# Kernel tuning notes

Hardware: AMD Instinct MI355X
Metric: run time of the kernel (lower is better)

## Reference

```python
import jax, jax.numpy as jnp
import numpy as np

N = 100000
DIM = 128
E_A = 500000
E_D = 500000


def setup_inputs() -> dict:
    key = jax.random.key(0)
    ks = jax.random.split(key, 8)
    h = jax.random.normal(ks[0], (N, DIM), dtype=jnp.float32)
    a_idx = jax.random.randint(ks[1], (E_A, 3), 0, N, dtype=jnp.int64 if jax.config.jax_enable_x64 else jnp.int32)
    a_val = jax.random.uniform(ks[2], (E_A, 1), dtype=jnp.float32)
    d_idx = jax.random.randint(ks[3], (E_D, 4), 0, N, dtype=jnp.int64 if jax.config.jax_enable_x64 else jnp.int32)
    d_val = jax.random.uniform(ks[4], (E_D, 1), dtype=jnp.float32)
    # Linear weights stored as [in, out]; init ~ Kaiming-uniform-ish scale
    W_a = jax.random.normal(ks[5], (3 * DIM + 1, DIM), dtype=jnp.float32) * (1.0 / np.sqrt(3 * DIM + 1))
    b_a = jnp.zeros((DIM,), dtype=jnp.float32)
    W_d = jax.random.normal(ks[6], (4 * DIM + 1, DIM), dtype=jnp.float32) * (1.0 / np.sqrt(4 * DIM + 1))
    b_d = jnp.zeros((DIM,), dtype=jnp.float32)
    W_h = jax.random.normal(ks[7], (3 * DIM, DIM), dtype=jnp.float32) * (1.0 / np.sqrt(3 * DIM))
    b_h = jnp.zeros((DIM,), dtype=jnp.float32)
    return {"h": h, "a_idx": a_idx, "a_val": a_val, "d_idx": d_idx, "d_val": d_val,
            "W_a": W_a, "b_a": b_a, "W_d": W_d, "b_d": b_d, "W_h": W_h, "b_h": b_h}


def reference(h, a_idx, a_val, d_idx, d_val, W_a, b_a, W_d, b_d, W_h, b_h):
    n = h.shape[0]
    # angle messages: gather 3 node embeddings + scalar, Linear + SiLU, scatter to center node
    x_a = jnp.concatenate([h[a_idx[:, 0]], h[a_idx[:, 1]], h[a_idx[:, 2]], a_val], axis=-1)  # [E_a, 3d+1]
    m_ijk = jax.nn.silu(x_a @ W_a + b_a)  # [E_a, d]
    agg_a = jax.ops.segment_sum(m_ijk, a_idx[:, 1], num_segments=n)  # [N, d]
    # dihedral messages: gather 4 node embeddings + scalar
    x_d = jnp.concatenate([h[d_idx[:, 0]], h[d_idx[:, 1]], h[d_idx[:, 2]], h[d_idx[:, 3]], d_val], axis=-1)  # [E_d, 4d+1]
    m_ijkl = jax.nn.silu(x_d @ W_d + b_d)  # [E_d, d]
    agg_d = jax.ops.segment_sum(m_ijkl, d_idx[:, 1], num_segments=n)  # [N, d]
    # residual node update
    return h + jnp.concatenate([h, agg_a, agg_d], axis=-1) @ W_h + b_h
```

## Files before the change

### kernel.cpp

```cpp
#include <hip/hip_runtime.h>
#include <hip/hip_bf16.h>

#define DIM 128
#define LDS_STRIDE 136
#define SC_STRIDE 132

typedef __attribute__((ext_vector_type(8))) __bf16 bf16x8;
typedef __attribute__((ext_vector_type(4))) __bf16 bf16x4;
typedef __attribute__((ext_vector_type(2))) __bf16 bf16x2;
typedef __attribute__((ext_vector_type(4))) float f32x4;

__global__ __launch_bounds__(256) void prep_w(const float* __restrict__ W_a,
                                              const float* __restrict__ W_d,
                                              const float* __restrict__ W_h,
                                              __bf16* __restrict__ Wt)
{
    int idx = blockIdx.x * 256 + threadIdx.x;
    if (idx >= 10 * 16384) return;
    int t   = idx >> 14;
    int rem = idx & 16383;
    int c   = rem >> 7;
    int k   = rem & 127;
    const float* src;
    if (t < 3)      src = W_a + (size_t)t * 16384;
    else if (t < 7) src = W_d + (size_t)(t - 3) * 16384;
    else            src = W_h + (size_t)(t - 7) * 16384;
    Wt[(size_t)t * 16384 + c * 128 + k] = (__bf16)src[k * 128 + c];
}

__device__ __forceinline__ void stage_wt(const __bf16* __restrict__ Wtj,
                                         __bf16 (*sB)[LDS_STRIDE], int tid)
{
    for (int it = 0; it < 8; ++it) {
        int idx = tid + it * 256;
        int c  = idx >> 4;
        int k8 = (idx & 15) << 3;
        *(bf16x8*)&sB[c][k8] = *(const bf16x8*)(Wtj + c * 128 + k8);
    }
}

__device__ __forceinline__ void load_afrag_f32(const float* __restrict__ src,
                                               int row, int lk, int N, bf16x8 afrag[4])
{
    const float* rp = src + (size_t)row * DIM;
    #pragma unroll
    for (int ks = 0; ks < 4; ++ks) {
        float4 v0 = make_float4(0.f, 0.f, 0.f, 0.f), v1 = v0;
        if (row < N) {
            v0 = *(const float4*)(rp + ks * 32 + lk);
            v1 = *(const float4*)(rp + ks * 32 + lk + 4);
        }
        bf16x8 a;
        a[0] = (__bf16)v0.x; a[1] = (__bf16)v0.y; a[2] = (__bf16)v0.z; a[3] = (__bf16)v0.w;
        a[4] = (__bf16)v1.x; a[5] = (__bf16)v1.y; a[6] = (__bf16)v1.z; a[7] = (__bf16)v1.w;
        afrag[ks] = a;
    }
}

__device__ __forceinline__ void load_afrag_bf16(const __bf16* __restrict__ src,
                                                int row, int lk, int N, bf16x8 afrag[4])
{
    const __bf16* rp = src + (size_t)row * DIM;
    #pragma unroll
    for (int ks = 0; ks < 4; ++ks) {
        bf16x8 a = {};
        if (row < N) a = *(const bf16x8*)(rp + ks * 32 + lk);
        afrag[ks] = a;
    }
}

__global__ __launch_bounds__(256, 4) void proj(const float* __restrict__ src,
                                               const __bf16* __restrict__ Wt,
                                               __bf16* __restrict__ dst,
                                               int N)
{
    __shared__ __bf16 sB[128][LDS_STRIDE];
    float* sC = reinterpret_cast<float*>(sB);
    const int tid = threadIdx.x;
    const int j = blockIdx.y;
    const int node0 = blockIdx.x * 64;
    const int wave = tid >> 6, lane = tid & 63;
    const int lrow = lane & 15;
    const int lk   = (lane >> 4) * 8;
    const int arow = node0 + wave * 16 + lrow;

    stage_wt(Wt + (size_t)j * 16384, sB, tid);

    bf16x8 afrag[4];
    load_afrag_f32(src, arow, lk, N, afrag);
    __syncthreads();

    f32x4 acc[8];
    #pragma unroll
    for (int ct = 0; ct < 8; ++ct) acc[ct] = (f32x4){0.f, 0.f, 0.f, 0.f};

    #pragma unroll
    for (int ks = 0; ks < 4; ++ks) {
        int k0 = ks * 32 + lk;
        #pragma unroll
        for (int ct = 0; ct < 8; ++ct) {
            bf16x8 b = *(const bf16x8*)&sB[ct * 16 + lrow][k0];
            acc[ct] = __builtin_amdgcn_mfma_f32_16x16x32_bf16(afrag[ks], b, acc[ct], 0, 0, 0);
        }
    }

    __syncthreads();
    {
        int rbase = wave * 16 + (lane >> 4) * 4;
        #pragma unroll
        for (int r = 0; r < 4; ++r)
            #pragma unroll
            for (int ct = 0; ct < 8; ++ct)
                sC[(rbase + r) * SC_STRIDE + ct * 16 + lrow] = acc[ct][r];
    }
    __syncthreads();

    __bf16* dj = dst + (size_t)j * N * DIM;
    for (int it = 0; it < 8; ++it) {
        int idx = tid + it * 256;
        int row = idx >> 5;
        int c4  = (idx & 31) << 2;
        int grow = node0 + row;
        if (grow < N) {
            const float* sp = sC + row * SC_STRIDE + c4;
            bf16x4 o;
            o[0] = (__bf16)sp[0]; o[1] = (__bf16)sp[1];
            o[2] = (__bf16)sp[2]; o[3] = (__bf16)sp[3];
            *(bf16x4*)(dj + (size_t)grow * DIM + c4) = o;
        }
    }
}

__global__ __launch_bounds__(256) void csr_count_both(const int* __restrict__ a_idx,
                                                      const int* __restrict__ d_idx,
                                                      int* __restrict__ offs,
                                                      int EA, int ED, int N)
{
    int e = blockIdx.x * 256 + threadIdx.x;
    if (e < EA) {
        atomicAdd(&offs[a_idx[3 * (size_t)e + 1]], 1);
    } else if (e < EA + ED) {
        int k = e - EA;
        atomicAdd(&offs[N + d_idx[4 * (size_t)k + 1]], 1);
    }
}

#define SCAN_CHUNK 1024

__global__ __launch_bounds__(256) void scan_s1(int* __restrict__ data,
                                               int* __restrict__ partials, int n)
{
    __shared__ int lds[256];
    const int t = threadIdx.x;
    const int base = blockIdx.x * SCAN_CHUNK + t * 4;
    int v[4];
    #pragma unroll
    for (int i = 0; i < 4; ++i) v[i] = (base + i < n) ? data[base + i] : 0;
    int tsum = v[0] + v[1] + v[2] + v[3];
    lds[t] = tsum; __syncthreads();
    for (int off = 1; off < 256; off <<= 1) {
        int x = (t >= off) ? lds[t - off] : 0;
        __syncthreads();
        lds[t] += x;
        __syncthreads();
    }
    if (t == 255) partials[blockIdx.x] = lds[255];
    int run = lds[t] - tsum;
    #pragma unroll
    for (int i = 0; i < 4; ++i) {
        int nv = run; run += v[i];
        if (base + i < n) data[base + i] = nv;
    }
}

__global__ __launch_bounds__(256) void scan_s2(int* __restrict__ partials, int nb)
{
    __shared__ int lds[256];
    const int t = threadIdx.x;
    int v = (t < nb) ? partials[t] : 0;
    lds[t] = v; __syncthreads();
    for (int off = 1; off < 256; off <<= 1) {
        int x = (t >= off) ? lds[t - off] : 0;
        __syncthreads();
        lds[t] += x;
        __syncthreads();
    }
    if (t < nb) partials[t] = lds[t] - v;
}

__global__ __launch_bounds__(256) void scan_s3(int* __restrict__ data,
                                               const int* __restrict__ partials, int n)
{
    const int add = partials[blockIdx.x];
    const int base = blockIdx.x * SCAN_CHUNK + threadIdx.x * 4;
    #pragma unroll
    for (int i = 0; i < 4; ++i)
        if (base + i < n) data[base + i] += add;
}

__global__ __launch_bounds__(256) void csr_fill_both(const int* __restrict__ a_idx,
                                                     const float* __restrict__ a_val,
                                                     const int* __restrict__ d_idx,
                                                     const float* __restrict__ d_val,
                                                     int* __restrict__ offs,
                                                     int4* __restrict__ recs,
                                                     int EA, int ED, int N)
{
    int e = blockIdx.x * 256 + threadIdx.x;
    if (e < EA) {
        int i0 = a_idx[3 * (size_t)e + 0];
        int i1 = a_idx[3 * (size_t)e + 1];
        int i2 = a_idx[3 * (size_t)e + 2];
        int slot = atomicAdd(&offs[i1], 1);
        recs[slot] = make_int4(i0 * 256, i2 * 256, __float_as_int(a_val[e]), 0);
    } else if (e < EA + ED) {
        int k = e - EA;
        int i0 = d_idx[4 * (size_t)k + 0];
        int i1 = d_idx[4 * (size_t)k + 1];
        int i2 = d_idx[4 * (size_t)k + 2];
        int i3 = d_idx[4 * (size_t)k + 3];
        int slot = atomicAdd(&offs[N + i1], 1);
        recs[slot] = make_int4(i0 * 256, i2 * 256, i3 * 256, __float_as_int(d_val[k]));
    }
}

__device__ __forceinline__ float silu(float x) { return x / (1.f + __expf(-x)); }

__global__ __launch_bounds__(256) void gather3(const __bf16* __restrict__ P,
                                               const float* __restrict__ wlast,
                                               const float* __restrict__ bias,
                                               const int* __restrict__ offs,
                                               const int4* __restrict__ recs,
                                               float* __restrict__ aggf, int N)
{
    const int tid = threadIdx.x;
    const int n = blockIdx.x * 4 + (tid >> 6);
    if (n >= N) return;
    const int lane = tid & 63;
    const int half = lane >> 5;
    const int gl = lane & 31;
    const int f  = gl * 4;
    const int fb = gl * 8;
    const size_t NBb = (size_t)N * DIM * 2;
    const char* P0b = (const char*)P;
    const char* P1b = P0b + NBb;
    const char* P2b = P0b + 2 * NBb;
    int start = (n == 0) ? 0 : offs[n - 1];
    int end = offs[n];

    float wl[4], base[4];
    {
        const float* wp = wlast + f;
        const float* bp = bias + f;
        bf16x4 p1 = *(const bf16x4*)(P1b + (size_t)n * 256 + fb);
        #pragma unroll
        for (int c = 0; c < 4; ++c) { wl[c] = wp[c]; base[c] = (float)p1[c] + bp[c]; }
    }
    float a[4] = {0.f, 0.f, 0.f, 0.f};

    const int cnt = end - start;
    const int npair = cnt >> 1;
    int s = start;
    for (int p = 0; p < npair; ++p, s += 2) {
        int4 r = recs[s + half];
        bf16x4 q0 = *(const bf16x4*)(P0b + r.x + fb);
        bf16x4 q2 = *(const bf16x4*)(P2b + r.y + fb);
        float v = __int_as_float(r.z);
        #pragma unroll
        for (int c = 0; c < 4; ++c)
            a[c] += silu((float)q0[c] + (float)q2[c] + v * wl[c] + base[c]);
    }
    if (cnt & 1) {
        int4 r = recs[end - 1];
        bf16x4 q0 = *(const bf16x4*)(P0b + r.x + fb);
        bf16x4 q2 = *(const bf16x4*)(P2b + r.y + fb);
        float v = __int_as_float(r.z);
        if (half == 0) {
            #pragma unroll
            for (int c = 0; c < 4; ++c)
                a[c] += silu((float)q0[c] + (float)q2[c] + v * wl[c] + base[c]);
        }
    }
    #pragma unroll
    for (int c = 0; c < 4; ++c) a[c] += __shfl_xor(a[c], 32, 64);
    if (half == 0) {
        f32x4 o;
        #pragma unroll
        for (int c = 0; c < 4; ++c) o[c] = a[c];
        *(f32x4*)(aggf + (size_t)n * DIM + f) = o;
    }
}

__global__ __launch_bounds__(256) void gather4(const __bf16* __restrict__ P,
                                               const float* __restrict__ wlast,
                                               const float* __restrict__ bias,
                                               const int* __restrict__ offs_d,
                                               const int4* __restrict__ recs,
                                               __bf16* __restrict__ agg, int N)
{
    const int tid = threadIdx.x;
    const int n = blockIdx.x * 4 + (tid >> 6);
    if (n >= N) return;
    const int lane = tid & 63;
    const int half = lane >> 5;
    const int gl = lane & 31;
    const int f  = gl * 4;
    const int fb = gl * 8;
    const size_t NBb = (size_t)N * DIM * 2;
    const char* P0b = (const char*)P;
    const char* P1b = P0b + NBb;
    const char* P2b = P0b + 2 * NBb;
    const char* P3b = P0b + 3 * NBb;
    int start = offs_d[n - 1];
    int end = offs_d[n];

    float wl[4], base[4];
    {
        const float* wp = wlast + f;
        const float* bp = bias + f;
        bf16x4 p1 = *(const bf16x4*)(P1b + (size_t)n * 256 + fb);
        #pragma unroll
        for (int c = 0; c < 4; ++c) { wl[c] = wp[c]; base[c] = (float)p1[c] + bp[c]; }
    }
    float a[4] = {0.f, 0.f, 0.f, 0.f};

    const int cnt = end - start;
    const int npair = cnt >> 1;
    int s = start;
    for (int p = 0; p < npair; ++p, s += 2) {
        int4 r = recs[s + half];
        bf16x4 q0 = *(const bf16x4*)(P0b + r.x + fb);
        bf16x4 q2 = *(const bf16x4*)(P2b + r.y + fb);
        bf16x4 q3 = *(const bf16x4*)(P3b + r.z + fb);
        float v = __int_as_float(r.w);
        #pragma unroll
        for (int c = 0; c < 4; ++c)
            a[c] += silu((float)q0[c] + (float)q2[c] + (float)q3[c] + v * wl[c] + base[c]);
    }
    if (cnt & 1) {
        int4 r = recs[end - 1];
        bf16x4 q0 = *(const bf16x4*)(P0b + r.x + fb);
        bf16x4 q2 = *(const bf16x4*)(P2b + r.y + fb);
        bf16x4 q3 = *(const bf16x4*)(P3b + r.z + fb);
        float v = __int_as_float(r.w);
        if (half == 0) {
            #pragma unroll
            for (int c = 0; c < 4; ++c)
                a[c] += silu((float)q0[c] + (float)q2[c] + (float)q3[c] + v * wl[c] + base[c]);
        }
    }
    #pragma unroll
    for (int c = 0; c < 4; ++c) a[c] += __shfl_xor(a[c], 32, 64);
    if (half == 0) {
        bf16x4 o;
        #pragma unroll
        for (int c = 0; c < 4; ++c) o[c] = (__bf16)a[c];
        *(bf16x4*)(agg + (size_t)n * DIM + f) = o;
    }
}

__global__ __launch_bounds__(256, 4) void update3(const float* __restrict__ h,
                                                  const float* __restrict__ aggA,
                                                  const __bf16* __restrict__ aggD,
                                                  const __bf16* __restrict__ Wt,
                                                  const float* __restrict__ bh,
                                                  float* __restrict__ out, int N)
{
    __shared__ __bf16 sB[128][LDS_STRIDE];
    float* sC = reinterpret_cast<float*>(sB);
    const int tid = threadIdx.x;
    const int node0 = blockIdx.x * 64;
    const int wave = tid >> 6, lane = tid & 63;
    const int lrow = lane & 15;
    const int lk   = (lane >> 4) * 8;
    const int arow = node0 + wave * 16 + lrow;

    f32x4 acc[8];
    #pragma unroll
    for (int ct = 0; ct < 8; ++ct) acc[ct] = (f32x4){0.f, 0.f, 0.f, 0.f};

    #pragma unroll
    for (int s = 0; s < 3; ++s) {
        __syncthreads();
        stage_wt(Wt + (size_t)s * 16384, sB, tid);

        bf16x8 afrag[4];
        if (s == 0)      load_afrag_f32(h,    arow, lk, N, afrag);
        else if (s == 1) load_afrag_f32(aggA, arow, lk, N, afrag);
        else             load_afrag_bf16(aggD, arow, lk, N, afrag);
        __syncthreads();

        #pragma unroll
        for (int ks = 0; ks < 4; ++ks) {
            int k0 = ks * 32 + lk;
            #pragma unroll
            for (int ct = 0; ct < 8; ++ct) {
                bf16x8 b = *(const bf16x8*)&sB[ct * 16 + lrow][k0];
                acc[ct] = __builtin_amdgcn_mfma_f32_16x16x32_bf16(afrag[ks], b, acc[ct], 0, 0, 0);
            }
        }
    }

    __syncthreads();
    {
        int rbase = wave * 16 + (lane >> 4) * 4;
        #pragma unroll
        for (int r = 0; r < 4; ++r)
            #pragma unroll
            for (int ct = 0; ct < 8; ++ct)
                sC[(rbase + r) * SC_STRIDE + ct * 16 + lrow] = acc[ct][r];
    }
    __syncthreads();

    for (int it = 0; it < 8; ++it) {
        int idx = tid + it * 256;
        int row = idx >> 5;
        int c4  = (idx & 31) << 2;
        int grow = node0 + row;
        if (grow < N) {
            const float* sp = sC + row * SC_STRIDE + c4;
            float4 rv = *(const float4*)(h + (size_t)grow * DIM + c4);
            float4 bv = *(const float4*)(bh + c4);
            float4 ov;
            ov.x = rv.x + bv.x + sp[0];
            ov.y = rv.y + bv.y + sp[1];
            ov.z = rv.z + bv.z + sp[2];
            ov.w = rv.w + bv.w + sp[3];
            *(float4*)(out + (size_t)grow * DIM + c4) = ov;
        }
    }
}

static inline size_t align16(size_t x) { return (x + 15) & ~(size_t)15; }

extern "C" void kernel_launch(void* const* d_in, const int* in_sizes, int n_in,
                              void* d_out, int out_size, void* d_ws, size_t ws_size,
                              hipStream_t stream)
{
    const float* h     = (const float*)d_in[0];
    const int*   a_idx = (const int*)d_in[1];
    const float* a_val = (const float*)d_in[2];
    const int*   d_idx = (const int*)d_in[3];
    const float* d_val = (const float*)d_in[4];
    const float* W_a   = (const float*)d_in[5];
    const float* b_a   = (const float*)d_in[6];
    const float* W_d   = (const float*)d_in[7];
    const float* b_d   = (const float*)d_in[8];
    const float* W_h   = (const float*)d_in[9];
    const float* b_h   = (const float*)d_in[10];
    float* out = (float*)d_out;

    const int N  = in_sizes[0] / DIM;
    const int EA = in_sizes[2];
    const int ED = in_sizes[4];
    const size_t NB = (size_t)N * DIM;
    const int twoN = 2 * N;
    const int NBLK = (twoN + SCAN_CHUNK - 1) / SCAN_CHUNK;

    size_t off = 0;
    __bf16* P    = (__bf16*)((char*)d_ws + off); off = align16(off + 4 * NB * sizeof(__bf16));
    __bf16* aggD = (__bf16*)((char*)d_ws + off); off = align16(off + NB * sizeof(__bf16));
    int* offs     = (int*)((char*)d_ws + off);  off = align16(off + (size_t)twoN * sizeof(int));
    int* partials = (int*)((char*)d_ws + off);  off = align16(off + 256 * sizeof(int));
    int4* recs    = (int4*)((char*)d_ws + off); off = align16(off + (size_t)(EA + ED) * sizeof(int4));
    __bf16* Wt  = (__bf16*)((char*)d_ws + off); off = align16(off + (size_t)10 * 16384 * sizeof(__bf16));
    if (ws_size < off) return;

    const int NT64 = (N + 63) / 64;
    const int GE = (EA + ED + 255) / 256;
    const int GN4 = (N + 3) / 4;

    prep_w<<<(10 * 16384 + 255) / 256, 256, 0, stream>>>(W_a, W_d, W_h, Wt);

    hipMemsetAsync(offs, 0, (size_t)twoN * sizeof(int), stream);
    csr_count_both<<<GE, 256, 0, stream>>>(a_idx, d_idx, offs, EA, ED, N);
    scan_s1<<<NBLK, 256, 0, stream>>>(offs, partials, twoN);
    scan_s2<<<1, 256, 0, stream>>>(partials, NBLK);
    scan_s3<<<NBLK, 256, 0, stream>>>(offs, partials, twoN);
    csr_fill_both<<<GE, 256, 0, stream>>>(a_idx, a_val, d_idx, d_val, offs, recs, EA, ED, N);

    {
        dim3 g(NT64, 3);
        proj<<<g, 256, 0, stream>>>(h, Wt, P, N);
    }
    gather3<<<GN4, 256, 0, stream>>>(P, W_a + 384 * DIM, b_a, offs, recs, out, N);

    {
        dim3 g(NT64, 4);
        proj<<<g, 256, 0, stream>>>(h, Wt + (size_t)3 * 16384, P, N);
    }
    gather4<<<GN4, 256, 0, stream>>>(P, W_d + 512 * DIM, b_d, offs + N, recs, aggD, N);

    update3<<<NT64, 256, 0, stream>>>(h, out, aggD, Wt + (size_t)7 * 16384, b_h, out, N);
}
```

Baseline: 378.6 us.

## Pre-convert h to bf16 and fold h@W_h projection into the batched proj launch

Adds a kernel that converts h to bf16 once into the output buffer, so every projection slice reads half the bytes and skips the per-slice f32 conversion. The launch order is swapped so dihedral runs first. The angle projection launch gains a fourth slice that computes h@W_h[0:128] into the spare P slot. The final update kernel then does only two K-slices and adds that precomputed bf16 term. This costs an extra conversion pass and rounds the h·W_h term to bf16 before it is added to the output.

```diff
diff --git a/kernel.cpp b/kernel.cpp
--- a/kernel.cpp
+++ b/kernel.cpp
@@ -7,7 +7,6 @@
 
 typedef __attribute__((ext_vector_type(8))) __bf16 bf16x8;
 typedef __attribute__((ext_vector_type(4))) __bf16 bf16x4;
-typedef __attribute__((ext_vector_type(2))) __bf16 bf16x2;
 typedef __attribute__((ext_vector_type(4))) float f32x4;
 
 __global__ __launch_bounds__(256) void prep_w(const float* __restrict__ W_a,
@@ -22,10 +21,23 @@
     int c   = rem >> 7;
     int k   = rem & 127;
     const float* src;
-    if (t < 3)      src = W_a + (size_t)t * 16384;
-    else if (t < 7) src = W_d + (size_t)(t - 3) * 16384;
+    if (t < 4)      src = W_d + (size_t)t * 16384;
+    else if (t < 7) src = W_a + (size_t)(t - 4) * 16384;
     else            src = W_h + (size_t)(t - 7) * 16384;
     Wt[(size_t)t * 16384 + c * 128 + k] = (__bf16)src[k * 128 + c];
+}
+
+__global__ __launch_bounds__(256) void h2bf(const float* __restrict__ h,
+                                            __bf16* __restrict__ hb, int n)
+{
+    int i = (blockIdx.x * 256 + threadIdx.x) * 8;
+    if (i >= n) return;
+    float4 v0 = *(const float4*)(h + i);
+    float4 v1 = *(const float4*)(h + i + 4);
+    bf16x8 o;
+    o[0] = (__bf16)v0.x; o[1] = (__bf16)v0.y; o[2] = (__bf16)v0.z; o[3] = (__bf16)v0.w;
+    o[4] = (__bf16)v1.x; o[5] = (__bf16)v1.y; o[6] = (__bf16)v1.z; o[7] = (__bf16)v1.w;
+    *(bf16x8*)(hb + i) = o;
 }
 
 __device__ __forceinline__ void stage_wt(const __bf16* __restrict__ Wtj,
@@ -69,7 +81,7 @@
     }
 }
 
-__global__ __launch_bounds__(256, 4) void proj(const float* __restrict__ src,
+__global__ __launch_bounds__(256, 4) void proj(const __bf16* __restrict__ src,
                                                const __bf16* __restrict__ Wt,
                                                __bf16* __restrict__ dst,
                                                int N)
@@ -87,7 +99,7 @@
     stage_wt(Wt + (size_t)j * 16384, sB, tid);
 
     bf16x8 afrag[4];
-    load_afrag_f32(src, arow, lk, N, afrag);
+    load_afrag_bf16(src, arow, lk, N, afrag);
     __syncthreads();
 
     f32x4 acc[8];
@@ -359,9 +371,10 @@
     }
 }
 
-__global__ __launch_bounds__(256, 4) void update3(const float* __restrict__ h,
+__global__ __launch_bounds__(256, 4) void update2(const float* __restrict__ h,
                                                   const float* __restrict__ aggA,
                                                   const __bf16* __restrict__ aggD,
+                                                  const __bf16* __restrict__ PH,
                                                   const __bf16* __restrict__ Wt,
                                                   const float* __restrict__ bh,
                                                   float* __restrict__ out, int N)
@@ -375,19 +388,18 @@
     const int lk   = (lane >> 4) * 8;
     const int arow = node0 + wave * 16 + lrow;
 
+    bf16x8 aA[4], aD[4];
+    load_afrag_f32(aggA, arow, lk, N, aA);
+    load_afrag_bf16(aggD, arow, lk, N, aD);
+
     f32x4 acc[8];
     #pragma unroll
     for (int ct = 0; ct < 8; ++ct) acc[ct] = (f32x4){0.f, 0.f, 0.f, 0.f};
 
     #pragma unroll
-    for (int s = 0; s < 3; ++s) {
+    for (int s = 0; s < 2; ++s) {
         __syncthreads();
         stage_wt(Wt + (size_t)s * 16384, sB, tid);
-
-        bf16x8 afrag[4];
-        if (s == 0)      load_afrag_f32(h,    arow, lk, N, afrag);
-        else if (s == 1) load_afrag_f32(aggA, arow, lk, N, afrag);
-        else             load_afrag_bf16(aggD, arow, lk, N, afrag);
         __syncthreads();
 
         #pragma unroll
@@ -396,7 +408,8 @@
             #pragma unroll
             for (int ct = 0; ct < 8; ++ct) {
                 bf16x8 b = *(const bf16x8*)&sB[ct * 16 + lrow][k0];
-                acc[ct] = __builtin_amdgcn_mfma_f32_16x16x32_bf16(afrag[ks], b, acc[ct], 0, 0, 0);
+                bf16x8 af = (s == 0) ? aA[ks] : aD[ks];
+                acc[ct] = __builtin_amdgcn_mfma_f32_16x16x32_bf16(af, b, acc[ct], 0, 0, 0);
             }
         }
     }
@@ -421,11 +434,12 @@
             const float* sp = sC + row * SC_STRIDE + c4;
             float4 rv = *(const float4*)(h + (size_t)grow * DIM + c4);
             float4 bv = *(const float4*)(bh + c4);
+            bf16x4 pv = *(const bf16x4*)(PH + (size_t)grow * DIM + c4);
             float4 ov;
-            ov.x = rv.x + bv.x + sp[0];
-            ov.y = rv.y + bv.y + sp[1];
-            ov.z = rv.z + bv.z + sp[2];
-            ov.w = rv.w + bv.w + sp[3];
+            ov.x = rv.x + bv.x + (float)pv[0] + sp[0];
+            ov.y = rv.y + bv.y + (float)pv[1] + sp[1];
+            ov.z = rv.z + bv.z + (float)pv[2] + sp[2];
+            ov.w = rv.w + bv.w + (float)pv[3] + sp[3];
             *(float4*)(out + (size_t)grow * DIM + c4) = ov;
         }
     }
@@ -470,7 +484,10 @@
     const int GE = (EA + ED + 255) / 256;
     const int GN4 = (N + 3) / 4;
 
+    __bf16* h_bf = (__bf16*)d_out;
+
     prep_w<<<(10 * 16384 + 255) / 256, 256, 0, stream>>>(W_a, W_d, W_h, Wt);
+    h2bf<<<(int)(NB / 8 + 255) / 256, 256, 0, stream>>>(h, h_bf, (int)NB);
 
     hipMemsetAsync(offs, 0, (size_t)twoN * sizeof(int), stream);
     csr_count_both<<<GE, 256, 0, stream>>>(a_idx, d_idx, offs, EA, ED, N);
@@ -480,16 +497,17 @@
     csr_fill_both<<<GE, 256, 0, stream>>>(a_idx, a_val, d_idx, d_val, offs, recs, EA, ED, N);
 
     {
-        dim3 g(NT64, 3);
-        proj<<<g, 256, 0, stream>>>(h, Wt, P, N);
-    }
-    gather3<<<GN4, 256, 0, stream>>>(P, W_a + 384 * DIM, b_a, offs, recs, out, N);
+        dim3 g(NT64, 4);
+        proj<<<g, 256, 0, stream>>>(h_bf, Wt, P, N);
+    }
+    gather4<<<GN4, 256, 0, stream>>>(P, W_d + 512 * DIM, b_d, offs + N, recs, aggD, N);
 
     {
         dim3 g(NT64, 4);
-        proj<<<g, 256, 0, stream>>>(h, Wt + (size_t)3 * 16384, P, N);
-    }
-    gather4<<<GN4, 256, 0, stream>>>(P, W_d + 512 * DIM, b_d, offs + N, recs, aggD, N);
-
-    update3<<<NT64, 256, 0, stream>>>(h, out, aggD, Wt + (size_t)7 * 16384, b_h, out, N);
-}
+        proj<<<g, 256, 0, stream>>>(h_bf, Wt + (size_t)4 * 16384, P, N);
+    }
+    gather3<<<GN4, 256, 0, stream>>>(P, W_a + 384 * DIM, b_a, offs, recs, out, N);
+
+    update2<<<NT64, 256, 0, stream>>>(h, out, aggD, P + 3 * NB, Wt + (size_t)8 * 16384,
+                                      b_h, out, N);
+}
```

Measured after the change: 354.6 us. 1.07x faster.
